# Performance work log

Measured on AMD Instinct MI355X. Metric: run time of the kernel, lower is better.

## Reference

```python
import jax, jax.numpy as jnp
import numpy as np

B, S, D = 2, 2048, 1024
H, DH, DM = 16, 64, 4096
EPS = 1e-5
IGNORE = -100000.0


def setup_inputs() -> dict:
    key = jax.random.key(0)
    ks = jax.random.split(key, 14)
    s = 0.02
    return {
        "x": jax.random.normal(ks[0], (B, S, D), jnp.float32),
        "W_Q": jax.random.normal(ks[1], (H, DH, D), jnp.float32) * s,
        "W_K": jax.random.normal(ks[2], (H, DH, D), jnp.float32) * s,
        "W_V": jax.random.normal(ks[3], (H, DH, D), jnp.float32) * s,
        "W_O": jax.random.normal(ks[4], (H, D, DH), jnp.float32) * s,
        "b_Q": jax.random.normal(ks[5], (H, DH), jnp.float32) * s,
        "b_K": jax.random.normal(ks[6], (H, DH), jnp.float32) * s,
        "b_V": jax.random.normal(ks[7], (H, DH), jnp.float32) * s,
        "b_O": jax.random.normal(ks[8], (D,), jnp.float32) * s,
        "W_in": jax.random.normal(ks[9], (DM, D), jnp.float32) * s,
        "b_in": jax.random.normal(ks[10], (DM,), jnp.float32) * s,
        "W_out": jax.random.normal(ks[11], (D, DM), jnp.float32) * s,
        "b_out": jax.random.normal(ks[12], (D,), jnp.float32) * s,
    }


def ln_pre(x):
    x = x - jnp.mean(x, axis=-1, keepdims=True)
    scale = jnp.sqrt(jnp.mean(x * x, axis=-1, keepdims=True) + EPS)
    return x / scale


def gelu_new(x):
    c = np.sqrt(2.0 / np.pi).astype(np.float32)
    return 0.5 * x * (1.0 + jnp.tanh(c * (x + 0.044715 * x ** 3)))


def reference(x, W_Q, W_K, W_V, W_O, b_Q, b_K, b_V, b_O, W_in, b_in, W_out, b_out):
    resid_pre = x
    xn = ln_pre(resid_pre)
    # q,k,v: [B, S, H, DH]
    q = jnp.einsum('ihm,bpm->bpih', W_Q, xn) + b_Q
    k = jnp.einsum('ihm,bpm->bpih', W_K, xn) + b_K
    v = jnp.einsum('ihm,bpm->bpih', W_V, xn) + b_V
    attn_scale = np.sqrt(DH).astype(np.float32)
    # scores: [B, H, Sq, Sk]  (einsum 'bpih,bqih->bipq')
    scores = jnp.einsum('bpih,bqih->bipq', q, k) / attn_scale
    mask = jnp.tril(jnp.ones((S, S), bool))
    scores = jnp.where(mask, scores, IGNORE)
    attn = jax.nn.softmax(scores, axis=-1)
    # z: [B, Sq, H, DH]
    z = jnp.einsum('bpih,biqp->bqih', v, attn)
    attn_out = jnp.einsum('idh,bqih->bqd', W_O, z) + b_O
    resid_mid = resid_pre + attn_out
    m = ln_pre(resid_mid)
    pre = jnp.einsum('md,bpd->bpm', W_in, m) + b_in
    post = gelu_new(pre)
    mlp_out = jnp.einsum('dm,bpm->bpd', W_out, post) + b_out
    return resid_mid + mlp_out
```

## Files before the change

kernel.cpp:

```cpp
#include <hip/hip_runtime.h>

typedef unsigned short u16;
typedef __attribute__((ext_vector_type(8))) short short8;
typedef __attribute__((ext_vector_type(4))) unsigned short ushort4v;
typedef __attribute__((ext_vector_type(4))) float float4v;

__device__ __forceinline__ float bf2f(u16 u) {
  union { unsigned int i; float f; } c; c.i = ((unsigned int)u) << 16; return c.f;
}
__device__ __forceinline__ u16 f2bf(float f) {
  union { float f; unsigned int i; } c; c.f = f;
  unsigned int u = c.i;
  return (u16)((u + 0x7fffu + ((u >> 16) & 1u)) >> 16);
}
__device__ __forceinline__ unsigned int cvt_pk_bf16(float a, float b) {
  unsigned int r;
  asm("v_cvt_pk_bf16_f32 %0, %1, %2" : "=v"(r) : "v"(a), "v"(b));
  return r;
}
__device__ __forceinline__ float gelu_new(float x) {
  const float k1 = 2.30218776f;
  const float k3 = 0.10294233f;
  float x3 = x * x * x;
  float e = __builtin_amdgcn_exp2f(-(k1 * x + k3 * x3));
  return x / (1.0f + e);
}
__device__ __forceinline__ float ldres(const float* p) { return *p; }
__device__ __forceinline__ float ldres(const u16* p) { return bf2f(*p); }

__device__ __forceinline__ void gload_lds16(const u16* g, u16* l) {
  __builtin_amdgcn_global_load_lds(
      (const __attribute__((address_space(1))) unsigned int*)g,
      (__attribute__((address_space(3))) unsigned int*)l, 16, 0, 0);
}

__global__ void cvt_bf16_multi(const float* __restrict__ s0, const float* __restrict__ s1,
                               const float* __restrict__ s2, const float* __restrict__ s3,
                               const float* __restrict__ s4, u16* __restrict__ d0,
                               u16* __restrict__ d1, u16* __restrict__ d2,
                               u16* __restrict__ d3, u16* __restrict__ d4) {
  int bid = blockIdx.x;
  const float* src; u16* dst; int base;
  if (bid < 512)       { src = s0; dst = d0; base = 0; }
  else if (bid < 1024) { src = s1; dst = d1; base = 512; }
  else if (bid < 1536) { src = s2; dst = d2; base = 1024; }
  else if (bid < 3584) { src = s3; dst = d3; base = 1536; }
  else                 { src = s4; dst = d4; base = 3584; }
  int t = (bid - base) * 256 + threadIdx.x;
  float4v a = *(const float4v*)(src + (size_t)t * 8);
  float4v b = *(const float4v*)(src + (size_t)t * 8 + 4);
  short8 o;
#pragma unroll
  for (int j = 0; j < 4; ++j) o[j] = (short)f2bf(a[j]);
#pragma unroll
  for (int j = 0; j < 4; ++j) o[4 + j] = (short)f2bf(b[j]);
  *(short8*)(dst + (size_t)t * 8) = o;
}

__global__ void prep_wo(const float* __restrict__ WO, u16* __restrict__ Wot) {
  int t = blockIdx.x * 256 + threadIdx.x;
  int i = t >> 13;
  int d = (t >> 3) & 1023;
  int h0 = (t & 7) * 8;
  const float* src = WO + (size_t)i * 65536 + d * 64 + h0;
  float4v a = *(const float4v*)(src);
  float4v b = *(const float4v*)(src + 4);
  short8 o;
#pragma unroll
  for (int j = 0; j < 4; ++j) o[j] = (short)f2bf(a[j]);
#pragma unroll
  for (int j = 0; j < 4; ++j) o[4 + j] = (short)f2bf(b[j]);
  *(short8*)(Wot + (size_t)d * 1024 + i * 64 + h0) = o;
}

__global__ void prep_bqkv(const float* __restrict__ bQ, const float* __restrict__ bK,
                          const float* __restrict__ bV, float* __restrict__ bqkv) {
  int t = blockIdx.x * 256 + threadIdx.x;
  if (t < 3072)
    bqkv[t] = (t < 1024) ? bQ[t] : (t < 2048) ? bK[t - 1024] : bV[t - 2048];
}

__global__ void ln_f32(const float* __restrict__ x, u16* __restrict__ y) {
  __shared__ float red1[4];
  __shared__ float red2[4];
  int token = blockIdx.x;
  int tid = threadIdx.x;
  int w = tid >> 6;
  const float* xr = x + (size_t)token * 1024;
  float4v v = *(const float4v*)(xr + tid * 4);
  float s = v[0] + v[1] + v[2] + v[3];
#pragma unroll
  for (int m = 32; m >= 1; m >>= 1) s += __shfl_xor(s, m);
  if ((tid & 63) == 0) red1[w] = s;
  __syncthreads();
  float mean = (red1[0] + red1[1] + red1[2] + red1[3]) * (1.0f / 1024.0f);
  float ss = 0.0f;
#pragma unroll
  for (int j = 0; j < 4; ++j) { v[j] -= mean; ss += v[j] * v[j]; }
#pragma unroll
  for (int m = 32; m >= 1; m >>= 1) ss += __shfl_xor(ss, m);
  if ((tid & 63) == 0) red2[w] = ss;
  __syncthreads();
  float ms = (red2[0] + red2[1] + red2[2] + red2[3]) * (1.0f / 1024.0f);
  float inv = 1.0f / sqrtf(ms + 1e-5f);
  ushort4v o;
#pragma unroll
  for (int j = 0; j < 4; ++j) o[j] = f2bf(v[j] * inv);
  *(ushort4v*)(y + (size_t)token * 1024 + tid * 4) = o;
}

__global__ void reduce_mlp(float* __restrict__ out, const u16* __restrict__ p1,
                           const u16* __restrict__ p2, const u16* __restrict__ p3) {
  size_t t = (size_t)blockIdx.x * 256 + threadIdx.x;
  float4v o0 = *(float4v*)(out + t * 8);
  float4v o1 = *(float4v*)(out + t * 8 + 4);
  short8 a = *(const short8*)(p1 + t * 8);
  short8 b = *(const short8*)(p2 + t * 8);
  short8 c = *(const short8*)(p3 + t * 8);
#pragma unroll
  for (int j = 0; j < 4; ++j)
    o0[j] += bf2f((u16)a[j]) + bf2f((u16)b[j]) + bf2f((u16)c[j]);
#pragma unroll
  for (int j = 0; j < 4; ++j)
    o1[j] += bf2f((u16)a[4 + j]) + bf2f((u16)b[4 + j]) + bf2f((u16)c[4 + j]);
  *(float4v*)(out + t * 8) = o0;
  *(float4v*)(out + t * 8 + 4) = o1;
}

template <int BN, int BK, bool GELU, bool VSPLIT, bool DBUF, typename TO, typename TR>
__global__ __launch_bounds__(256) void gemm_bt(
    const u16* __restrict__ A, const u16* __restrict__ Bw,
    const float* __restrict__ bias, const TR* __restrict__ resid,
    TO* __restrict__ C, u16* __restrict__ vTout, int M, int N, int K,
    int lda, int ldc) {
  constexpr int BM = 128;
  constexpr int SEGS = BK / 8;
  constexpr int SMASK = SEGS - 1;
  constexpr int FI = 4, FJ = BN / 32;
  constexpr int CA = BM * SEGS / 256;
  constexpr int CB = BN * SEGS / 256;
  constexpr int NB = DBUF ? 2 : 1;
  __shared__ __align__(16) u16 As[NB][BM * BK];
  __shared__ __align__(16) u16 Bs[NB][BN * BK];
  const int tid = threadIdx.x;
  const int w = tid >> 6, lane = tid & 63;
  const int quad = lane >> 4, l16 = lane & 15;
  const int m0 = blockIdx.x * BM, n0 = blockIdx.y * BN;
  const int wm = (w >> 1) * 64, wn = (w & 1) * (BN / 2);
  const int rmask = l16 & SMASK;
  float4v acc[FI][FJ] = {};

  auto stage = [&](int buf, int k0) {
#pragma unroll
    for (int t = 0; t < CA; ++t) {
      int chunk = (w * CA + t) * 64 + lane;
      int row = chunk / SEGS, seg = chunk % SEGS;
      int sseg = seg ^ (row & SMASK);
      gload_lds16(A + (size_t)(m0 + row) * lda + k0 + sseg * 8,
                  As[buf] + (w * CA + t) * 512);
    }
#pragma unroll
    for (int t = 0; t < CB; ++t) {
      int chunk = (w * CB + t) * 64 + lane;
      int row = chunk / SEGS, seg = chunk % SEGS;
      int sseg = seg ^ (row & SMASK);
      gload_lds16(Bw + (size_t)(n0 + row) * K + k0 + sseg * 8,
                  Bs[buf] + (w * CB + t) * 512);
    }
  };
  auto compute = [&](int buf) {
#pragma unroll
    for (int kk = 0; kk < BK; kk += 32) {
      short8 a[FI], b[FJ];
#pragma unroll
      for (int fi = 0; fi < FI; ++fi)
        a[fi] = *(const short8*)(As[buf] + (wm + fi * 16 + l16) * BK +
                                 ((((kk >> 3) + quad) ^ rmask) << 3));
#pragma unroll
      for (int fj = 0; fj < FJ; ++fj)
        b[fj] = *(const short8*)(Bs[buf] + (wn + fj * 16 + l16) * BK +
                                 ((((kk >> 3) + quad) ^ rmask) << 3));
#pragma unroll
      for (int fi = 0; fi < FI; ++fi)
#pragma unroll
        for (int fj = 0; fj < FJ; ++fj)
          acc[fi][fj] = __builtin_amdgcn_mfma_f32_16x16x32_bf16(
              a[fi], b[fj], acc[fi][fj], 0, 0, 0);
    }
  };

  if constexpr (DBUF) {
    stage(0, 0);
    __syncthreads();
    int cur = 0;
    for (int k0 = 0; k0 < K; k0 += BK) {
      if (k0 + BK < K) stage(cur ^ 1, k0 + BK);
      compute(cur);
      __syncthreads();
      cur ^= 1;
    }
  } else {
    for (int k0 = 0; k0 < K; k0 += BK) {
      __syncthreads();
      stage(0, k0);
      __syncthreads();
      compute(0);
    }
  }

#pragma unroll
  for (int fi = 0; fi < FI; ++fi) {
#pragma unroll
    for (int fj = 0; fj < FJ; ++fj) {
      int col = n0 + wn + fj * 16 + l16;
      float bv = bias ? bias[col] : 0.0f;
#pragma unroll
      for (int r = 0; r < 4; ++r) {
        int row = m0 + wm + fi * 16 + quad * 4 + r;
        float val = acc[fi][fj][r] + bv;
        if (resid) val += ldres(resid + (size_t)row * N + col);
        if (GELU) val = gelu_new(val);
        if (VSPLIT && col < 1024) val *= 0.18033688011112042f;
        if (VSPLIT && col >= 2048) {
          vTout[(size_t)(col - 2048) * 4096 + row] = f2bf(val);
        } else if constexpr (sizeof(TO) == 2) {
          C[(size_t)row * ldc + col] = f2bf(val);
        } else {
          C[(size_t)row * ldc + col] = val;
        }
      }
    }
  }
}

template <bool GELU, bool SPLITK>
__global__ __launch_bounds__(1024, 4) void gemm256k(
    const u16* __restrict__ A, const u16* __restrict__ Bw,
    const float* __restrict__ bias, const float* __restrict__ resid,
    float* __restrict__ outF, u16* __restrict__ outB,
    u16* __restrict__ p1, u16* __restrict__ p2, u16* __restrict__ p3,
    int lda, int ldb, int ldc) {
  constexpr int BK = 32;
  __shared__ __align__(16) u16 As[3][256 * BK];
  __shared__ __align__(16) u16 Bs[3][256 * BK];
  const int tid = threadIdx.x;
  const int w = tid >> 6, lane = tid & 63;
  const int quad = lane >> 4, l16 = lane & 15;
  const int rmask = l16 & 3;
  int mt, nt;
  if constexpr (SPLITK) {
    mt = blockIdx.x >> 2; nt = blockIdx.x & 3;
  } else {
    const int id = blockIdx.x;
    const int xcd = id & 7, local = id >> 3;
    mt = (xcd & 3) * 4 + (local >> 3);
    nt = (xcd >> 2) * 8 + (local & 7);
  }
  const int m0 = mt * 256, n0 = nt * 256;
  const int wm = (w >> 2) * 64, wn = (w & 3) * 64;
  const int kBase = SPLITK ? blockIdx.y * 1024 : 0;

  const int srow = tid >> 2, spos = tid & 3;
  const int sseg = spos ^ (srow & 3);
  const u16* aSrc = A + (size_t)(m0 + srow) * lda + kBase + sseg * 8;
  const u16* bSrc = Bw + (size_t)(n0 + srow) * ldb + kBase + sseg * 8;

  float4v acc[4][4] = {};

  auto stage = [&](int buf, int t) {
    gload_lds16(aSrc + t * BK, &As[buf][tid * 8]);
    gload_lds16(bSrc + t * BK, &Bs[buf][tid * 8]);
  };
  auto compute = [&](int buf) {
    short8 a_[4], b_[4];
#pragma unroll
    for (int mi = 0; mi < 4; ++mi)
      a_[mi] = *(const short8*)(&As[buf][(wm + mi * 16 + l16) * BK +
                                         ((quad ^ rmask) << 3)]);
#pragma unroll
    for (int ni = 0; ni < 4; ++ni)
      b_[ni] = *(const short8*)(&Bs[buf][(wn + ni * 16 + l16) * BK +
                                         ((quad ^ rmask) << 3)]);
    __builtin_amdgcn_s_setprio(1);
#pragma unroll
    for (int mi = 0; mi < 4; ++mi)
#pragma unroll
      for (int ni = 0; ni < 4; ++ni)
        acc[mi][ni] = __builtin_amdgcn_mfma_f32_16x16x32_bf16(
            a_[mi], b_[ni], acc[mi][ni], 0, 0, 0);
    __builtin_amdgcn_s_setprio(0);
  };

  constexpr int ntk = 32;
  stage(0, 0);
  stage(1, 1);
  stage(2, 2);
  asm volatile("s_waitcnt vmcnt(4)" ::: "memory");
  asm volatile("s_barrier" ::: "memory");

  int buf = 0;
  for (int t = 0; t < ntk; ++t) {
    compute(buf);
    if (t == ntk - 1) break;
    asm volatile("s_waitcnt lgkmcnt(0)" ::: "memory");
    asm volatile("s_barrier" ::: "memory");
    if (t + 3 < ntk) {
      stage(buf, t + 3);
      asm volatile("s_waitcnt vmcnt(4)" ::: "memory");
    } else if (t + 2 < ntk) {
      asm volatile("s_waitcnt vmcnt(2)" ::: "memory");
    } else {
      asm volatile("s_waitcnt vmcnt(0)" ::: "memory");
    }
    asm volatile("s_barrier" ::: "memory");
    buf = (buf == 2) ? 0 : buf + 1;
  }

#pragma unroll
  for (int mi = 0; mi < 4; ++mi) {
#pragma unroll
    for (int ni = 0; ni < 4; ++ni) {
      int col = n0 + wn + ni * 16 + l16;
#pragma unroll
      for (int r = 0; r < 4; ++r) {
        int row = m0 + wm + mi * 16 + quad * 4 + r;
        float val = acc[mi][ni][r];
        if constexpr (SPLITK) {
          if (blockIdx.y == 0) {
            outF[(size_t)row * ldc + col] =
                val + bias[col] + resid[(size_t)row * ldc + col];
          } else {
            u16* pz = (blockIdx.y == 1) ? p1 : (blockIdx.y == 2) ? p2 : p3;
            pz[(size_t)row * ldc + col] = f2bf(val);
          }
        } else {
          val += bias[col];
          if (GELU) val = gelu_new(val);
          outB[(size_t)row * ldc + col] = f2bf(val);
        }
      }
    }
  }
}

__global__ __launch_bounds__(256) void attn_flash(u16* __restrict__ qk,
                                                  const u16* __restrict__ vT) {
  constexpr int PADK = 72;
  constexpr float THR2 = 10.0f;
  __shared__ __align__(16) u16 Ks[64 * PADK];
  __shared__ __align__(16) u16 Vt[64 * PADK];
  __shared__ __align__(16) u16 Ps[4][16 * PADK];
  const int id = blockIdx.x;
  const int qt = 31 - (id >> 5);
  const int combo = id & 31;
  const int head = combo >> 1, b = combo & 1;
  const int tid = threadIdx.x;
  const int w = tid >> 6, lane = tid & 63;
  const int quad = lane >> 4, l16 = lane & 15;
  const int q0 = qt * 64;
  const size_t tokB = (size_t)b * 2048;

  short8 aq[2];
#pragma unroll
  for (int ks = 0; ks < 2; ++ks)
    aq[ks] = *(const short8*)(qk + (tokB + q0 + w * 16 + l16) * 2048 +
                              head * 64 + ks * 32 + quad * 8);

  const u16* kbase = qk + tokB * 2048 + 1024 + head * 64;
  const u16* vbase = vT + (size_t)head * 64 * 4096 + tokB;

  short8 bones = {};
  if (l16 == 0) {
#pragma unroll
    for (int j = 0; j < 8; ++j) bones[j] = (short)0x3F80;
  }

  float m_st[4] = {-1e30f, -1e30f, -1e30f, -1e30f};
  float4v o_acc[4] = {};
  float4v o5 = {0.f, 0.f, 0.f, 0.f};

  const int srow = tid >> 2;
  const int sseg = (tid & 3) * 2;
  const u16* kptr = kbase + (size_t)srow * 2048 + sseg * 8;
  const u16* vptr = vbase + (size_t)srow * 4096 + sseg * 8;
  u16* ksl = Ks + srow * PADK + sseg * 8;
  u16* vsl = Vt + srow * PADK + sseg * 8;

  short8 pk0 = *(const short8*)(kptr);
  short8 pk1 = *(const short8*)(kptr + 8);
  short8 pv0 = *(const short8*)(vptr);
  short8 pv1 = *(const short8*)(vptr + 8);

  for (int kt = 0; kt <= qt; ++kt) {
    const int kk0 = kt * 64;
    __syncthreads();
    *(short8*)(ksl) = pk0;
    *(short8*)(ksl + 8) = pk1;
    *(short8*)(vsl) = pv0;
    *(short8*)(vsl + 8) = pv1;
    __syncthreads();
    if (kt < qt) {
      const u16* kp = kptr + (size_t)(kk0 + 64) * 2048;
      const u16* vp = vptr + kk0 + 64;
      pk0 = *(const short8*)(kp);
      pk1 = *(const short8*)(kp + 8);
      pv0 = *(const short8*)(vp);
      pv1 = *(const short8*)(vp + 8);
    }

    float4v s[4];
    __builtin_amdgcn_s_setprio(1);
#pragma unroll
    for (int fj = 0; fj < 4; ++fj) {
      float4v t = {0.f, 0.f, 0.f, 0.f};
#pragma unroll
      for (int ks = 0; ks < 2; ++ks) {
        short8 bk = *(const short8*)(Ks + (fj * 16 + l16) * PADK + ks * 32 + quad * 8);
        t = __builtin_amdgcn_mfma_f32_16x16x32_bf16(aq[ks], bk, t, 0, 0, 0);
      }
      s[fj] = t;
    }
    __builtin_amdgcn_s_setprio(0);
    if (kt == qt) {
#pragma unroll
      for (int fj = 0; fj < 4; ++fj) {
        int col = kk0 + fj * 16 + l16;
#pragma unroll
        for (int r = 0; r < 4; ++r) {
          int row = q0 + w * 16 + quad * 4 + r;
          if (col > row) s[fj][r] = -1e30f;
        }
      }
    }
    float mx[4];
#pragma unroll
    for (int r = 0; r < 4; ++r) {
      float m = fmaxf(fmaxf(s[0][r], s[1][r]), fmaxf(s[2][r], s[3][r]));
      m = fmaxf(m, __shfl_xor(m, 1));
      m = fmaxf(m, __shfl_xor(m, 2));
      m = fmaxf(m, __shfl_xor(m, 4));
      m = fmaxf(m, __shfl_xor(m, 8));
      mx[r] = m;
    }
    bool need = false;
#pragma unroll
    for (int r = 0; r < 4; ++r) need |= (mx[r] > m_st[r] + THR2);
    if (__any(need)) {
#pragma unroll
      for (int r = 0; r < 4; ++r) {
        float mnew = fmaxf(m_st[r], mx[r]);
        float al = __builtin_amdgcn_exp2f(m_st[r] - mnew);
        m_st[r] = mnew;
        o5[r] *= al;
#pragma unroll
        for (int fj = 0; fj < 4; ++fj) o_acc[fj][r] *= al;
      }
    }
#pragma unroll
    for (int fj = 0; fj < 4; ++fj) {
#pragma unroll
      for (int r = 0; r < 4; r += 2) {
        float e0 = __builtin_amdgcn_exp2f(s[fj][r] - m_st[r]);
        float e1 = __builtin_amdgcn_exp2f(s[fj][r + 1] - m_st[r + 1]);
        unsigned int pp = cvt_pk_bf16(e0, e1);
        Ps[w][(quad * 4 + r) * PADK + fj * 16 + l16] = (u16)pp;
        Ps[w][(quad * 4 + r + 1) * PADK + fj * 16 + l16] = (u16)(pp >> 16);
      }
    }
    short8 ap[2];
#pragma unroll
    for (int ks = 0; ks < 2; ++ks)
      ap[ks] = *(const short8*)(&Ps[w][l16 * PADK + ks * 32 + quad * 8]);
    __builtin_amdgcn_s_setprio(1);
#pragma unroll
    for (int fj = 0; fj < 4; ++fj)
#pragma unroll
      for (int ks = 0; ks < 2; ++ks) {
        short8 bv = *(const short8*)(Vt + (fj * 16 + l16) * PADK + ks * 32 + quad * 8);
        o_acc[fj] = __builtin_amdgcn_mfma_f32_16x16x32_bf16(ap[ks], bv, o_acc[fj], 0, 0, 0);
      }
#pragma unroll
    for (int ks = 0; ks < 2; ++ks)
      o5 = __builtin_amdgcn_mfma_f32_16x16x32_bf16(ap[ks], bones, o5, 0, 0, 0);
    __builtin_amdgcn_s_setprio(0);
  }
#pragma unroll
  for (int r = 0; r < 4; ++r) {
    float lsum = __shfl(o5[r], lane & 48);
    float inv = 1.0f / lsum;
    int row = q0 + w * 16 + quad * 4 + r;
#pragma unroll
    for (int fj = 0; fj < 4; ++fj)
      qk[(tokB + row) * 2048 + head * 64 + fj * 16 + l16] =
          f2bf(o_acc[fj][r] * inv);
  }
}

extern "C" void kernel_launch(void* const* d_in, const int* in_sizes, int n_in,
                              void* d_out, int out_size, void* d_ws, size_t ws_size,
                              hipStream_t stream) {
  const float* x = (const float*)d_in[0];
  const float* W_Q = (const float*)d_in[1];
  const float* W_K = (const float*)d_in[2];
  const float* W_V = (const float*)d_in[3];
  const float* W_O = (const float*)d_in[4];
  const float* b_Q = (const float*)d_in[5];
  const float* b_K = (const float*)d_in[6];
  const float* b_V = (const float*)d_in[7];
  const float* b_O = (const float*)d_in[8];
  const float* W_in = (const float*)d_in[9];
  const float* b_in = (const float*)d_in[10];
  const float* W_out = (const float*)d_in[11];
  const float* b_out = (const float*)d_in[12];
  float* out = (float*)d_out;

  char* ws = (char*)d_ws;
  u16* Wqkv = (u16*)(ws);
  u16* Wot  = (u16*)(ws + 6291456);
  u16* Wib  = (u16*)(ws + 8388608);
  u16* Wob  = (u16*)(ws + 16777216);
  float* bqkv = (float*)(ws + 25165824);
  u16* xn   = (u16*)(ws + 25178112);
  u16* qk   = (u16*)(ws + 33566720);
  u16* vT   = (u16*)(ws + 50343936);
  u16* hbuf = (u16*)(ws + 33566720);
  float* rm = (float*)(ws + 67121152);
  u16* P1 = (u16*)(ws);
  u16* P2 = (u16*)(ws + 8388608);
  u16* P3 = (u16*)(ws + 25178112);

  cvt_bf16_multi<<<5632, 256, 0, stream>>>(W_Q, W_K, W_V, W_in, W_out,
                                           Wqkv, Wqkv + 1048576, Wqkv + 2097152,
                                           Wib, Wob);
  prep_wo<<<512, 256, 0, stream>>>(W_O, Wot);
  prep_bqkv<<<12, 256, 0, stream>>>(b_Q, b_K, b_V, bqkv);

  ln_f32<<<4096, 256, 0, stream>>>(x, xn);
  gemm_bt<128, 64, false, true, false, u16, float><<<dim3(32, 24), 256, 0, stream>>>(
      xn, Wqkv, bqkv, (const float*)nullptr, qk, vT, 4096, 3072, 1024, 1024, 2048);
  attn_flash<<<1024, 256, 0, stream>>>(qk, vT);
  gemm_bt<64, 64, false, false, true, float, float><<<dim3(32, 16), 256, 0, stream>>>(
      qk , Wot, b_O, x, rm, nullptr, 4096, 1024, 1024, 2048, 1024);
  ln_f32<<<4096, 256, 0, stream>>>(rm, xn);
  gemm256k<true, false><<<dim3(256, 1), 1024, 0, stream>>>(
      xn, Wib, b_in, nullptr, nullptr, hbuf, nullptr, nullptr, nullptr,
      1024, 1024, 4096);
  gemm256k<false, true><<<dim3(64, 4), 1024, 0, stream>>>(
      hbuf, Wob, b_out, rm, out, nullptr, P1, P2, P3,
      4096, 4096, 1024);
  reduce_mlp<<<2048, 256, 0, stream>>>(out, P1, P2, P3);
}
```

Measured before the change: 365.6 us.

## Use 8-wave 256x256 MLP GEMM with 128x64 warp tiles and new swizzle

Runs the two MLP GEMMs with 512 threads (8 waves) per block instead of 1024, so each wave computes a 128x64 sub-tile with 8x4 MFMA accumulators. Each thread now issues two global-to-LDS loads per operand per stage, and the vmcnt waits are doubled to match. The LDS swizzle XORs two row-bit pairs to cut bank conflicts for the new access pattern. More register reuse per wave lowers LDS read traffic per MFMA, but the larger accumulator set raises register pressure and fewer waves are available to hide latency.

```diff
diff --git a/kernel.cpp b/kernel.cpp
--- a/kernel.cpp
+++ b/kernel.cpp
@@ -234,7 +234,7 @@
 }
 
 template <bool GELU, bool SPLITK>
-__global__ __launch_bounds__(1024, 4) void gemm256k(
+__global__ __launch_bounds__(512, 2) void gemm256s(
     const u16* __restrict__ A, const u16* __restrict__ Bw,
     const float* __restrict__ bias, const float* __restrict__ resid,
     float* __restrict__ outF, u16* __restrict__ outB,
@@ -246,7 +246,7 @@
   const int tid = threadIdx.x;
   const int w = tid >> 6, lane = tid & 63;
   const int quad = lane >> 4, l16 = lane & 15;
-  const int rmask = l16 & 3;
+  const int rm2 = (l16 & 3) ^ ((l16 >> 2) & 3);
   int mt, nt;
   if constexpr (SPLITK) {
     mt = blockIdx.x >> 2; nt = blockIdx.x & 3;
@@ -257,33 +257,43 @@
     nt = (xcd >> 2) * 8 + (local & 7);
   }
   const int m0 = mt * 256, n0 = nt * 256;
-  const int wm = (w >> 2) * 64, wn = (w & 3) * 64;
+  const int wm = (w >> 2) * 128, wn = (w & 3) * 64;
   const int kBase = SPLITK ? blockIdx.y * 1024 : 0;
 
-  const int srow = tid >> 2, spos = tid & 3;
-  const int sseg = spos ^ (srow & 3);
-  const u16* aSrc = A + (size_t)(m0 + srow) * lda + kBase + sseg * 8;
-  const u16* bSrc = Bw + (size_t)(n0 + srow) * ldb + kBase + sseg * 8;
-
-  float4v acc[4][4] = {};
+  const u16* aSrc[2];
+  const u16* bSrc[2];
+#pragma unroll
+  for (int i = 0; i < 2; ++i) {
+    int chunk = (w * 2 + i) * 64 + lane;
+    int row = chunk >> 2, pos = chunk & 3;
+    int sseg = pos ^ ((row & 3) ^ ((row >> 2) & 3));
+    aSrc[i] = A + (size_t)(m0 + row) * lda + kBase + sseg * 8;
+    bSrc[i] = Bw + (size_t)(n0 + row) * ldb + kBase + sseg * 8;
+  }
+
+  float4v acc[8][4] = {};
 
   auto stage = [&](int buf, int t) {
-    gload_lds16(aSrc + t * BK, &As[buf][tid * 8]);
-    gload_lds16(bSrc + t * BK, &Bs[buf][tid * 8]);
+#pragma unroll
+    for (int i = 0; i < 2; ++i)
+      gload_lds16(aSrc[i] + t * BK, &As[buf][(w * 2 + i) * 512]);
+#pragma unroll
+    for (int i = 0; i < 2; ++i)
+      gload_lds16(bSrc[i] + t * BK, &Bs[buf][(w * 2 + i) * 512]);
   };
   auto compute = [&](int buf) {
-    short8 a_[4], b_[4];
-#pragma unroll
-    for (int mi = 0; mi < 4; ++mi)
+    short8 a_[8], b_[4];
+#pragma unroll
+    for (int mi = 0; mi < 8; ++mi)
       a_[mi] = *(const short8*)(&As[buf][(wm + mi * 16 + l16) * BK +
-                                         ((quad ^ rmask) << 3)]);
+                                         ((quad ^ rm2) << 3)]);
 #pragma unroll
     for (int ni = 0; ni < 4; ++ni)
       b_[ni] = *(const short8*)(&Bs[buf][(wn + ni * 16 + l16) * BK +
-                                         ((quad ^ rmask) << 3)]);
+                                         ((quad ^ rm2) << 3)]);
     __builtin_amdgcn_s_setprio(1);
 #pragma unroll
-    for (int mi = 0; mi < 4; ++mi)
+    for (int mi = 0; mi < 8; ++mi)
 #pragma unroll
       for (int ni = 0; ni < 4; ++ni)
         acc[mi][ni] = __builtin_amdgcn_mfma_f32_16x16x32_bf16(
@@ -295,7 +305,7 @@
   stage(0, 0);
   stage(1, 1);
   stage(2, 2);
-  asm volatile("s_waitcnt vmcnt(4)" ::: "memory");
+  asm volatile("s_waitcnt vmcnt(8)" ::: "memory");
   asm volatile("s_barrier" ::: "memory");
 
   int buf = 0;
@@ -306,9 +316,9 @@
     asm volatile("s_barrier" ::: "memory");
     if (t + 3 < ntk) {
       stage(buf, t + 3);
+      asm volatile("s_waitcnt vmcnt(8)" ::: "memory");
+    } else if (t + 2 < ntk) {
       asm volatile("s_waitcnt vmcnt(4)" ::: "memory");
-    } else if (t + 2 < ntk) {
-      asm volatile("s_waitcnt vmcnt(2)" ::: "memory");
     } else {
       asm volatile("s_waitcnt vmcnt(0)" ::: "memory");
     }
@@ -317,7 +327,7 @@
   }
 
 #pragma unroll
-  for (int mi = 0; mi < 4; ++mi) {
+  for (int mi = 0; mi < 8; ++mi) {
 #pragma unroll
     for (int ni = 0; ni < 4; ++ni) {
       int col = n0 + wn + ni * 16 + l16;
@@ -542,10 +552,10 @@
   gemm_bt<64, 64, false, false, true, float, float><<<dim3(32, 16), 256, 0, stream>>>(
       qk , Wot, b_O, x, rm, nullptr, 4096, 1024, 1024, 2048, 1024);
   ln_f32<<<4096, 256, 0, stream>>>(rm, xn);
-  gemm256k<true, false><<<dim3(256, 1), 1024, 0, stream>>>(
+  gemm256s<true, false><<<dim3(256, 1), 512, 0, stream>>>(
       xn, Wib, b_in, nullptr, nullptr, hbuf, nullptr, nullptr, nullptr,
       1024, 1024, 4096);
-  gemm256k<false, true><<<dim3(64, 4), 1024, 0, stream>>>(
+  gemm256s<false, true><<<dim3(64, 4), 512, 0, stream>>>(
       hbuf, Wob, b_out, rm, out, nullptr, P1, P2, P3,
       4096, 4096, 1024);
   reduce_mlp<<<2048, 256, 0, stream>>>(out, P1, P2, P3);
```

Result: slower. 383.9 us (+5.0%).
